# Kernel tuning notes

Hardware: AMD Instinct MI355X
Metric: run time of the kernel (lower is better)

Reference implementation:

```python
import jax, jax.numpy as jnp
import numpy as np

N_NODES = 50000
N_EDGES = 600000
IN_DIM = 128
HID_DIM = 256
LAT_DIM = 64


def setup_inputs() -> dict:
    key = jax.random.key(0)
    k_x, k_e, k_w1, k_b1, k_w2, k_b2 = jax.random.split(key, 6)
    x = jax.random.normal(k_x, (N_NODES, IN_DIM), dtype=jnp.float32)
    edge_index = jax.random.randint(k_e, (2, N_EDGES), 0, N_NODES, dtype=jnp.int64)
    # torch nn.Linear default init: U(-1/sqrt(fan_in), 1/sqrt(fan_in))
    lim1 = 1.0 / np.sqrt(2 * IN_DIM)
    lim2 = 1.0 / np.sqrt(HID_DIM)
    W1 = jax.random.uniform(k_w1, (2 * IN_DIM, HID_DIM), jnp.float32, -lim1, lim1)
    b1 = jax.random.uniform(k_b1, (HID_DIM,), jnp.float32, -lim1, lim1)
    W2 = jax.random.uniform(k_w2, (HID_DIM, LAT_DIM), jnp.float32, -lim2, lim2)
    b2 = jax.random.uniform(k_b2, (LAT_DIM,), jnp.float32, -lim2, lim2)
    return {"x": x, "edge_index": edge_index, "W1": W1, "b1": b1, "W2": W2, "b2": b2}


def reference(x, edge_index, W1, b1, W2, b2):
    h_i = x[edge_index[0]]                     # [E, D]
    h_j = x[edge_index[1]]                     # [E, D]
    edge_features = jnp.concatenate([h_i, h_j], axis=-1)  # [E, 2D]
    hidden = jax.nn.relu(edge_features @ W1 + b1)          # [E, H]
    return hidden @ W2 + b2                                # [E, L]
```

## Files before the change

### kernel.cpp

```cpp
#include <hip/hip_runtime.h>

#define E_TOTAL 600000
#define N_NODES 50000
#define NETILES 9375
#define NNT 782
#define LDS_X 136
#define LDP 264

typedef __attribute__((ext_vector_type(8))) short short8;
typedef __attribute__((ext_vector_type(8))) _Float16 half8;
typedef __attribute__((ext_vector_type(4))) float f32x4;

__device__ __forceinline__ unsigned f2bf_u(float f) {
  union { float f; unsigned u; } v; v.f = f;
  return (v.u + 0x7fffu + ((v.u >> 16) & 1u)) >> 16;
}
__device__ __forceinline__ unsigned short f2h_u(float f) {
  union { _Float16 h; unsigned short u; } v; v.h = (_Float16)f;
  return v.u;
}

__global__ __launch_bounds__(256) void prep(
    const float* __restrict__ W1, const float* __restrict__ W2,
    const float* __restrict__ b1,
    unsigned short* __restrict__ W1c, unsigned short* __restrict__ W2t2,
    unsigned short* __restrict__ b1h) {
  __shared__ float t[32][33];
  int bid = blockIdx.x;
  int tx = threadIdx.x & 31, ty = threadIdx.x >> 5;
  if (bid < 64) {
    int k0 = (bid >> 3) * 32, n0 = (bid & 7) * 32;
#pragma unroll
    for (int i = 0; i < 32; i += 8) t[ty + i][tx] = W1[(k0 + ty + i) * 256 + n0 + tx];
    __syncthreads();
    int coff = (k0 >= 128) ? 256 : 0;
#pragma unroll
    for (int i = 0; i < 32; i += 8)
      W1c[(n0 + ty + i + coff) * 128 + (k0 & 127) + tx] = (unsigned short)f2bf_u(t[tx][ty + i]);
  } else if (bid < 80) {
    int b = bid - 64;
    int k0 = (b >> 1) * 32, n0 = (b & 1) * 32;
#pragma unroll
    for (int i = 0; i < 32; i += 8) t[ty + i][tx] = W2[(k0 + ty + i) * 64 + n0 + tx];
    __syncthreads();
#pragma unroll
    for (int i = 0; i < 32; i += 8)
      W2t2[(n0 + ty + i) * 256 + k0 + tx] = f2h_u(t[tx][ty + i]);
  } else {
    b1h[threadIdx.x] = f2h_u(b1[threadIdx.x]);
  }
}

__global__ __launch_bounds__(256, 3) void node_uv(
    const float* __restrict__ x, const unsigned short* __restrict__ W1c,
    unsigned short* __restrict__ UV) {
  __shared__ __align__(16) unsigned short xt[64 * LDP];
  const int tid = threadIdx.x;
  const int ntile = (int)blockIdx.x >> 1, chalf = blockIdx.x & 1;
  const int n0 = ntile * 64;
  const int lane = tid & 63, w = tid >> 6, m = lane & 15, q = lane >> 4;

  const int kb = (tid & 15) * 8;
  const int r0 = tid >> 4;
#pragma unroll
  for (int i = 0; i < 4; ++i) {
    int r = r0 + 16 * i;
    int n = n0 + r; if (n >= N_NODES) n = N_NODES - 1;
    const float* p = x + (size_t)n * 128 + kb;
    f32x4 g0 = *(const f32x4*)p, g1 = *(const f32x4*)(p + 4);
    short8 s;
#pragma unroll
    for (int j = 0; j < 4; ++j) { s[j] = (short)f2bf_u(g0[j]); s[4 + j] = (short)f2bf_u(g1[j]); }
    *(short8*)&xt[r * LDS_X + kb] = s;
  }

  int w1o[4];
#pragma unroll
  for (int nt = 0; nt < 4; ++nt) w1o[nt] = (chalf * 256 + (w * 4 + nt) * 16 + m) * 128 + q * 8;
  short8 wa[2][4];
#pragma unroll
  for (int nt = 0; nt < 4; ++nt) wa[0][nt] = *(const short8*)&W1c[w1o[nt]];

  __syncthreads();

  f32x4 acc[4][4];
#pragma unroll
  for (int nt = 0; nt < 4; ++nt)
#pragma unroll
    for (int mt = 0; mt < 4; ++mt) acc[nt][mt] = (f32x4){0.f, 0.f, 0.f, 0.f};

#pragma unroll
  for (int kk = 0; kk < 4; ++kk) {
    const int cur = kk & 1, nx = cur ^ 1;
    if (kk < 3) {
#pragma unroll
      for (int nt = 0; nt < 4; ++nt) wa[nx][nt] = *(const short8*)&W1c[w1o[nt] + (kk + 1) * 32];
    }
    short8 f[4];
#pragma unroll
    for (int mt = 0; mt < 4; ++mt)
      f[mt] = *(const short8*)&xt[(mt * 16 + m) * LDS_X + kk * 32 + q * 8];
#pragma unroll
    for (int nt = 0; nt < 4; ++nt)
#pragma unroll
      for (int mt = 0; mt < 4; ++mt)
        acc[nt][mt] = __builtin_amdgcn_mfma_f32_16x16x32_bf16(wa[cur][nt], f[mt], acc[nt][mt], 0, 0, 0);
  }

  __syncthreads();

#pragma unroll
  for (int nt = 0; nt < 4; ++nt)
#pragma unroll
    for (int mt = 0; mt < 4; ++mt) {
      union { _Float16 h[4]; uint2 u; } pk;
#pragma unroll
      for (int r = 0; r < 4; ++r) pk.h[r] = (_Float16)acc[nt][mt][r];
      *(uint2*)&xt[(mt * 16 + m) * LDP + (w * 4 + nt) * 16 + q * 4] = pk.u;
    }

  __syncthreads();

  const int rr = tid >> 2, c8 = tid & 3;
  if (n0 + rr < N_NODES) {
    unsigned short* dst = UV + (size_t)(n0 + rr) * 512 + chalf * 256;
#pragma unroll
    for (int i = 0; i < 8; ++i) {
      int ch = c8 + 4 * i;
      *(short8*)&dst[ch * 8] = *(const short8*)&xt[rr * LDP + ch * 8];
    }
  }
}

__global__ __launch_bounds__(256, 4) void edge_mlp(
    const unsigned short* __restrict__ UV, const int* __restrict__ ei,
    const unsigned short* __restrict__ W2t2, const unsigned short* __restrict__ b1h,
    const float* __restrict__ b2, float* __restrict__ out) {
  __shared__ __align__(16) unsigned short hid[64 * LDP];
  const int tid = threadIdx.x;
  const int base = blockIdx.x * 64;
  const int lane = tid & 63, w = tid >> 6, m = lane & 15, q = lane >> 4;
  const int c = tid & 31;
  const int e0 = tid >> 5;

  half8 w2r[8];
  const int w2off = (w * 16 + m) * 256 + q * 8;
#pragma unroll
  for (int kk = 0; kk < 8; ++kk) w2r[kk] = *(const half8*)&W2t2[w2off + kk * 32];
  half8 bias = *(const half8*)&b1h[c * 8];
  f32x4 b2v = *(const f32x4*)&b2[w * 16 + q * 4];

  int si[8], di[8];
#pragma unroll
  for (int i = 0; i < 8; ++i) {
    int e = base + e0 + 8 * i;
    si[i] = ei[e];
    di[i] = ei[E_TOTAL + e];
  }

#pragma unroll
  for (int g = 0; g < 2; ++g) {
    half8 lu[4], lv[4];
#pragma unroll
    for (int i = 0; i < 4; ++i) {
      const int r = g * 4 + i;
      lu[i] = *(const half8*)&UV[(size_t)si[r] * 512 + c * 8];
      lv[i] = *(const half8*)&UV[(size_t)di[r] * 512 + 256 + c * 8];
    }
#pragma unroll
    for (int i = 0; i < 4; ++i) {
      const int r = g * 4 + i;
      half8 s = lu[i] + lv[i] + bias;
#pragma unroll
      for (int j = 0; j < 8; ++j) s[j] = s[j] > (_Float16)0 ? s[j] : (_Float16)0;
      *(half8*)&hid[(e0 + 8 * r) * LDP + c * 8] = s;
    }
  }

  __syncthreads();

  f32x4 acc2[4];
#pragma unroll
  for (int mt = 0; mt < 4; ++mt) acc2[mt] = (f32x4){0.f, 0.f, 0.f, 0.f};
#pragma unroll
  for (int kk = 0; kk < 8; ++kk) {
#pragma unroll
    for (int mt = 0; mt < 4; ++mt) {
      half8 h = *(const half8*)&hid[(mt * 16 + m) * LDP + kk * 32 + q * 8];
      acc2[mt] = __builtin_amdgcn_mfma_f32_16x16x32_f16(w2r[kk], h, acc2[mt], 0, 0, 0);
    }
  }

#pragma unroll
  for (int mt = 0; mt < 4; ++mt) {
    f32x4 o;
#pragma unroll
    for (int r = 0; r < 4; ++r) o[r] = acc2[mt][r] + b2v[r];
    __builtin_nontemporal_store(o, (f32x4*)&out[(size_t)(base + mt * 16 + m) * 64 + w * 16 + q * 4]);
  }
}

extern "C" void kernel_launch(void* const* d_in, const int* in_sizes, int n_in,
                              void* d_out, int out_size, void* d_ws, size_t ws_size,
                              hipStream_t stream) {
  const float* x  = (const float*)d_in[0];
  const int*   ei = (const int*)d_in[1];
  const float* W1 = (const float*)d_in[2];
  const float* b1 = (const float*)d_in[3];
  const float* W2 = (const float*)d_in[4];
  const float* b2 = (const float*)d_in[5];
  float* out = (float*)d_out;

  unsigned short* W1c  = (unsigned short*)d_ws;
  unsigned short* W2t2 = W1c + 512 * 128;
  unsigned short* b1h  = W2t2 + 64 * 256;
  unsigned short* UV   = b1h + 256;

  prep<<<81, 256, 0, stream>>>(W1, W2, b1, W1c, W2t2, b1h);
  node_uv<<<NNT * 2, 256, 0, stream>>>(x, W1c, UV);
  edge_mlp<<<NETILES, 256, 0, stream>>>(UV, ei, W2t2, b1h, b2, out);
}
```

Baseline: 290.9 us.

## Sort edges by source node to improve gather locality in edge MLP

Adds a counting sort of edges by source node (histogram, single-block scan, atomic scatter) and makes the edge kernel process edges in sorted order, writing outputs back through a permutation index. U and V are split into separate contiguous arrays so each gather hits a denser buffer. The aim is better cache reuse of source-node U rows during the random gather. In exchange it adds three kernels, one of which is a serial single-block scan, plus atomics and scattered output stores.

```diff
diff --git a/kernel.cpp b/kernel.cpp
--- a/kernel.cpp
+++ b/kernel.cpp
@@ -24,7 +24,7 @@
     const float* __restrict__ W1, const float* __restrict__ W2,
     const float* __restrict__ b1,
     unsigned short* __restrict__ W1c, unsigned short* __restrict__ W2t2,
-    unsigned short* __restrict__ b1h) {
+    unsigned short* __restrict__ b1h, int* __restrict__ hist) {
   __shared__ float t[32][33];
   int bid = blockIdx.x;
   int tx = threadIdx.x & 31, ty = threadIdx.x >> 5;
@@ -46,14 +46,54 @@
 #pragma unroll
     for (int i = 0; i < 32; i += 8)
       W2t2[(n0 + ty + i) * 256 + k0 + tx] = f2h_u(t[tx][ty + i]);
+  } else if (bid == 80) {
+    b1h[threadIdx.x] = f2h_u(b1[threadIdx.x]);
   } else {
-    b1h[threadIdx.x] = f2h_u(b1[threadIdx.x]);
+    int i = (bid - 81) * 256 + threadIdx.x;
+    if (i < N_NODES) hist[i] = 0;
+  }
+}
+
+__global__ __launch_bounds__(256) void ehist(const int* __restrict__ ei, int* __restrict__ hist) {
+  int e = blockIdx.x * 256 + threadIdx.x;
+  if (e < E_TOTAL) atomicAdd(&hist[ei[e]], 1);
+}
+
+__global__ __launch_bounds__(256) void escan(const int* __restrict__ hist, int* __restrict__ offs) {
+  __shared__ int tmp[256];
+  const int t = threadIdx.x;
+  const int b = t * 196;
+  int s = 0;
+#pragma unroll 4
+  for (int i = 0; i < 196; ++i) { int idx = b + i; if (idx < N_NODES) s += hist[idx]; }
+  tmp[t] = s; __syncthreads();
+  for (int o = 1; o < 256; o <<= 1) {
+    int v = (t >= o) ? tmp[t - o] : 0;
+    __syncthreads();
+    tmp[t] += v;
+    __syncthreads();
+  }
+  int run = tmp[t] - s;
+  for (int i = 0; i < 196; ++i) {
+    int idx = b + i;
+    if (idx < N_NODES) { offs[idx] = run; run += hist[idx]; }
+  }
+}
+
+__global__ __launch_bounds__(256) void escatter(const int* __restrict__ ei, int* __restrict__ offs,
+                                                int* __restrict__ ss, int* __restrict__ sd,
+                                                int* __restrict__ se) {
+  int e = blockIdx.x * 256 + threadIdx.x;
+  if (e < E_TOTAL) {
+    int s = ei[e], d = ei[E_TOTAL + e];
+    int p = atomicAdd(&offs[s], 1);
+    ss[p] = s; sd[p] = d; se[p] = e;
   }
 }
 
 __global__ __launch_bounds__(256, 3) void node_uv(
     const float* __restrict__ x, const unsigned short* __restrict__ W1c,
-    unsigned short* __restrict__ UV) {
+    unsigned short* __restrict__ U, unsigned short* __restrict__ V) {
   __shared__ __align__(16) unsigned short xt[64 * LDP];
   const int tid = threadIdx.x;
   const int ntile = (int)blockIdx.x >> 1, chalf = blockIdx.x & 1;
@@ -123,7 +163,7 @@
 
   const int rr = tid >> 2, c8 = tid & 3;
   if (n0 + rr < N_NODES) {
-    unsigned short* dst = UV + (size_t)(n0 + rr) * 512 + chalf * 256;
+    unsigned short* dst = (chalf ? V : U) + (size_t)(n0 + rr) * 256;
 #pragma unroll
     for (int i = 0; i < 8; ++i) {
       int ch = c8 + 4 * i;
@@ -133,7 +173,8 @@
 }
 
 __global__ __launch_bounds__(256, 4) void edge_mlp(
-    const unsigned short* __restrict__ UV, const int* __restrict__ ei,
+    const unsigned short* __restrict__ U, const unsigned short* __restrict__ V,
+    const int* __restrict__ ss, const int* __restrict__ sd, const int* __restrict__ se,
     const unsigned short* __restrict__ W2t2, const unsigned short* __restrict__ b1h,
     const float* __restrict__ b2, float* __restrict__ out) {
   __shared__ __align__(16) unsigned short hid[64 * LDP];
@@ -153,9 +194,9 @@
   int si[8], di[8];
 #pragma unroll
   for (int i = 0; i < 8; ++i) {
-    int e = base + e0 + 8 * i;
-    si[i] = ei[e];
-    di[i] = ei[E_TOTAL + e];
+    int r = base + e0 + 8 * i;
+    si[i] = ss[r];
+    di[i] = sd[r];
   }
 
 #pragma unroll
@@ -164,8 +205,8 @@
 #pragma unroll
     for (int i = 0; i < 4; ++i) {
       const int r = g * 4 + i;
-      lu[i] = *(const half8*)&UV[(size_t)si[r] * 512 + c * 8];
-      lv[i] = *(const half8*)&UV[(size_t)di[r] * 512 + 256 + c * 8];
+      lu[i] = *(const half8*)&U[(size_t)si[r] * 256 + c * 8];
+      lv[i] = *(const half8*)&V[(size_t)di[r] * 256 + c * 8];
     }
 #pragma unroll
     for (int i = 0; i < 4; ++i) {
@@ -193,10 +234,11 @@
 
 #pragma unroll
   for (int mt = 0; mt < 4; ++mt) {
+    int eo = se[base + mt * 16 + m];
     f32x4 o;
 #pragma unroll
     for (int r = 0; r < 4; ++r) o[r] = acc2[mt][r] + b2v[r];
-    __builtin_nontemporal_store(o, (f32x4*)&out[(size_t)(base + mt * 16 + m) * 64 + w * 16 + q * 4]);
+    __builtin_nontemporal_store(o, (f32x4*)&out[(size_t)eo * 64 + w * 16 + q * 4]);
   }
 }
 
@@ -214,9 +256,18 @@
   unsigned short* W1c  = (unsigned short*)d_ws;
   unsigned short* W2t2 = W1c + 512 * 128;
   unsigned short* b1h  = W2t2 + 64 * 256;
-  unsigned short* UV   = b1h + 256;
-
-  prep<<<81, 256, 0, stream>>>(W1, W2, b1, W1c, W2t2, b1h);
-  node_uv<<<NNT * 2, 256, 0, stream>>>(x, W1c, UV);
-  edge_mlp<<<NETILES, 256, 0, stream>>>(UV, ei, W2t2, b1h, b2, out);
-}
+  unsigned short* U    = b1h + 256;
+  unsigned short* V    = U + (size_t)N_NODES * 256;
+  int* hist = (int*)(V + (size_t)N_NODES * 256);
+  int* offs = hist + N_NODES;
+  int* ss   = offs + N_NODES;
+  int* sd   = ss + E_TOTAL;
+  int* se   = sd + E_TOTAL;
+
+  prep<<<277, 256, 0, stream>>>(W1, W2, b1, W1c, W2t2, b1h, hist);
+  ehist<<<2344, 256, 0, stream>>>(ei, hist);
+  escan<<<1, 256, 0, stream>>>(hist, offs);
+  escatter<<<2344, 256, 0, stream>>>(ei, offs, ss, sd, se);
+  node_uv<<<NNT * 2, 256, 0, stream>>>(x, W1c, U, V);
+  edge_mlp<<<NETILES, 256, 0, stream>>>(U, V, ss, sd, se, W2t2, b1h, b2, out);
+}
```

After: 427.4 us. 46.9% more time.

## Bucket-sort edges by source node to improve gather locality in edge MLP

Applied to the files above, without the earlier changes.

Adds a histogram, a single-block scan and an atomic scatter that bucket edges by source node (groups of 32), so the edge MLP gathers U rows with better cache locality. It also splits UV into separate U and V arrays and processes three 64-edge tiles per block, prefetching the next tile's gathers while the current one is computed. Outputs are written to the original edge positions, which turns the store into a scatter. The cost is extra kernels, atomics and a sorted buffer. Packing src and dst into 16 bits each relies on node ids fitting in 16 bits, which holds for 50000.

```diff
diff --git a/kernel.cpp b/kernel.cpp
--- a/kernel.cpp
+++ b/kernel.cpp
@@ -2,8 +2,11 @@
 
 #define E_TOTAL 600000
 #define N_NODES 50000
-#define NETILES 9375
+#define NBUCK 1563
+#define EB 3
+#define NEB 3125
 #define NNT 782
+#define SCAT_B 2344
 #define LDS_X 136
 #define LDP 264
 
@@ -19,14 +22,22 @@
   union { _Float16 h; unsigned short u; } v; v.h = (_Float16)f;
   return v.u;
 }
-
-__global__ __launch_bounds__(256) void prep(
+__device__ __forceinline__ void ldsBarrier() {
+  asm volatile("s_waitcnt lgkmcnt(0)\n\ts_barrier" ::: "memory");
+}
+
+__global__ __launch_bounds__(256) void prep_hist(
     const float* __restrict__ W1, const float* __restrict__ W2,
-    const float* __restrict__ b1,
+    const float* __restrict__ b1, const int* __restrict__ ei,
     unsigned short* __restrict__ W1c, unsigned short* __restrict__ W2t2,
-    unsigned short* __restrict__ b1h) {
+    unsigned short* __restrict__ b1h, int* __restrict__ hist) {
   __shared__ float t[32][33];
   int bid = blockIdx.x;
+  if (bid >= 81) {
+    int e = (bid - 81) * 256 + threadIdx.x;
+    if (e < E_TOTAL) atomicAdd(&hist[ei[e] >> 5], 1);
+    return;
+  }
   int tx = threadIdx.x & 31, ty = threadIdx.x >> 5;
   if (bid < 64) {
     int k0 = (bid >> 3) * 32, n0 = (bid & 7) * 32;
@@ -51,12 +62,52 @@
   }
 }
 
-__global__ __launch_bounds__(256, 3) void node_uv(
+__global__ __launch_bounds__(256) void bscan(const int* __restrict__ hist,
+                                             int* __restrict__ offs) {
+  __shared__ int tmp[256];
+  const int t = threadIdx.x;
+  const int base = t * 7;
+  int loc[7];
+  int s = 0;
+#pragma unroll
+  for (int i = 0; i < 7; ++i) {
+    int idx = base + i;
+    int v = (idx < NBUCK) ? hist[idx] : 0;
+    loc[i] = s; s += v;
+  }
+  tmp[t] = s; __syncthreads();
+  for (int o = 1; o < 256; o <<= 1) {
+    int u = (t >= o) ? tmp[t - o] : 0;
+    __syncthreads();
+    tmp[t] += u;
+    __syncthreads();
+  }
+  int pre = tmp[t] - s;
+#pragma unroll
+  for (int i = 0; i < 7; ++i) {
+    int idx = base + i;
+    if (idx < NBUCK) offs[idx] = pre + loc[i];
+  }
+}
+
+__global__ __launch_bounds__(256, 3) void scat_node(
+    const int* __restrict__ ei, int* __restrict__ offs, uint2* __restrict__ sorted,
     const float* __restrict__ x, const unsigned short* __restrict__ W1c,
-    unsigned short* __restrict__ UV) {
+    unsigned short* __restrict__ U, unsigned short* __restrict__ V) {
+  const int tid = threadIdx.x;
+  int bid = blockIdx.x;
+  if (bid < SCAT_B) {
+    int e = bid * 256 + tid;
+    if (e < E_TOTAL) {
+      int s = ei[e], d = ei[E_TOTAL + e];
+      int p = atomicAdd(&offs[s >> 5], 1);
+      sorted[p] = make_uint2((unsigned)s | ((unsigned)d << 16), (unsigned)e);
+    }
+    return;
+  }
   __shared__ __align__(16) unsigned short xt[64 * LDP];
-  const int tid = threadIdx.x;
-  const int ntile = (int)blockIdx.x >> 1, chalf = blockIdx.x & 1;
+  bid -= SCAT_B;
+  const int ntile = bid >> 1, chalf = bid & 1;
   const int n0 = ntile * 64;
   const int lane = tid & 63, w = tid >> 6, m = lane & 15, q = lane >> 4;
 
@@ -123,7 +174,7 @@
 
   const int rr = tid >> 2, c8 = tid & 3;
   if (n0 + rr < N_NODES) {
-    unsigned short* dst = UV + (size_t)(n0 + rr) * 512 + chalf * 256;
+    unsigned short* dst = (chalf ? V : U) + (size_t)(n0 + rr) * 256;
 #pragma unroll
     for (int i = 0; i < 8; ++i) {
       int ch = c8 + 4 * i;
@@ -132,13 +183,13 @@
   }
 }
 
-__global__ __launch_bounds__(256, 4) void edge_mlp(
-    const unsigned short* __restrict__ UV, const int* __restrict__ ei,
+__global__ __launch_bounds__(256, 3) void edge_mlp(
+    const unsigned short* __restrict__ U, const unsigned short* __restrict__ V,
+    const uint2* __restrict__ sorted,
     const unsigned short* __restrict__ W2t2, const unsigned short* __restrict__ b1h,
     const float* __restrict__ b2, float* __restrict__ out) {
   __shared__ __align__(16) unsigned short hid[64 * LDP];
   const int tid = threadIdx.x;
-  const int base = blockIdx.x * 64;
   const int lane = tid & 63, w = tid >> 6, m = lane & 15, q = lane >> 4;
   const int c = tid & 31;
   const int e0 = tid >> 5;
@@ -150,53 +201,61 @@
   half8 bias = *(const half8*)&b1h[c * 8];
   f32x4 b2v = *(const f32x4*)&b2[w * 16 + q * 4];
 
-  int si[8], di[8];
+  const int base = blockIdx.x * (EB * 64);
+
+  half8 gu[8], gv[8];
 #pragma unroll
   for (int i = 0; i < 8; ++i) {
-    int e = base + e0 + 8 * i;
-    si[i] = ei[e];
-    di[i] = ei[E_TOTAL + e];
-  }
-
-#pragma unroll
-  for (int g = 0; g < 2; ++g) {
-    half8 lu[4], lv[4];
-#pragma unroll
-    for (int i = 0; i < 4; ++i) {
-      const int r = g * 4 + i;
-      lu[i] = *(const half8*)&UV[(size_t)si[r] * 512 + c * 8];
-      lv[i] = *(const half8*)&UV[(size_t)di[r] * 512 + 256 + c * 8];
-    }
-#pragma unroll
-    for (int i = 0; i < 4; ++i) {
-      const int r = g * 4 + i;
-      half8 s = lu[i] + lv[i] + bias;
-#pragma unroll
-      for (int j = 0; j < 8; ++j) s[j] = s[j] > (_Float16)0 ? s[j] : (_Float16)0;
-      *(half8*)&hid[(e0 + 8 * r) * LDP + c * 8] = s;
-    }
-  }
-
-  __syncthreads();
-
-  f32x4 acc2[4];
-#pragma unroll
-  for (int mt = 0; mt < 4; ++mt) acc2[mt] = (f32x4){0.f, 0.f, 0.f, 0.f};
-#pragma unroll
-  for (int kk = 0; kk < 8; ++kk) {
+    uint2 s8 = sorted[base + e0 + 8 * i];
+    gu[i] = *(const half8*)&U[(size_t)(s8.x & 0xFFFFu) * 256 + c * 8];
+    gv[i] = *(const half8*)&V[(size_t)(s8.x >> 16) * 256 + c * 8];
+  }
+
+  for (int j = 0; j < EB; ++j) {
+    const int tb = base + j * 64;
+
+#pragma unroll
+    for (int i = 0; i < 8; ++i) {
+      half8 s = gu[i] + gv[i] + bias;
+#pragma unroll
+      for (int jj = 0; jj < 8; ++jj) s[jj] = s[jj] > (_Float16)0 ? s[jj] : (_Float16)0;
+      *(half8*)&hid[(e0 + 8 * i) * LDP + c * 8] = s;
+    }
+
+    if (j + 1 < EB) {
+      const int nb = tb + 64;
+#pragma unroll
+      for (int i = 0; i < 8; ++i) {
+        uint2 s8 = sorted[nb + e0 + 8 * i];
+        gu[i] = *(const half8*)&U[(size_t)(s8.x & 0xFFFFu) * 256 + c * 8];
+        gv[i] = *(const half8*)&V[(size_t)(s8.x >> 16) * 256 + c * 8];
+      }
+    }
+
+    ldsBarrier();
+
+    f32x4 acc2[4];
+#pragma unroll
+    for (int mt = 0; mt < 4; ++mt) acc2[mt] = (f32x4){0.f, 0.f, 0.f, 0.f};
+#pragma unroll
+    for (int kk = 0; kk < 8; ++kk) {
+#pragma unroll
+      for (int mt = 0; mt < 4; ++mt) {
+        half8 h = *(const half8*)&hid[(mt * 16 + m) * LDP + kk * 32 + q * 8];
+        acc2[mt] = __builtin_amdgcn_mfma_f32_16x16x32_f16(w2r[kk], h, acc2[mt], 0, 0, 0);
+      }
+    }
+
 #pragma unroll
     for (int mt = 0; mt < 4; ++mt) {
-      half8 h = *(const half8*)&hid[(mt * 16 + m) * LDP + kk * 32 + q * 8];
-      acc2[mt] = __builtin_amdgcn_mfma_f32_16x16x32_f16(w2r[kk], h, acc2[mt], 0, 0, 0);
-    }
-  }
-
-#pragma unroll
-  for (int mt = 0; mt < 4; ++mt) {
-    f32x4 o;
-#pragma unroll
-    for (int r = 0; r < 4; ++r) o[r] = acc2[mt][r] + b2v[r];
-    __builtin_nontemporal_store(o, (f32x4*)&out[(size_t)(base + mt * 16 + m) * 64 + w * 16 + q * 4]);
+      unsigned eo = sorted[tb + mt * 16 + m].y;
+      f32x4 o;
+#pragma unroll
+      for (int r = 0; r < 4; ++r) o[r] = acc2[mt][r] + b2v[r];
+      __builtin_nontemporal_store(o, (f32x4*)&out[(size_t)eo * 64 + w * 16 + q * 4]);
+    }
+
+    ldsBarrier();
   }
 }
 
@@ -214,9 +273,15 @@
   unsigned short* W1c  = (unsigned short*)d_ws;
   unsigned short* W2t2 = W1c + 512 * 128;
   unsigned short* b1h  = W2t2 + 64 * 256;
-  unsigned short* UV   = b1h + 256;
-
-  prep<<<81, 256, 0, stream>>>(W1, W2, b1, W1c, W2t2, b1h);
-  node_uv<<<NNT * 2, 256, 0, stream>>>(x, W1c, UV);
-  edge_mlp<<<NETILES, 256, 0, stream>>>(UV, ei, W2t2, b1h, b2, out);
-}
+  unsigned short* U    = b1h + 256;
+  unsigned short* V    = U + (size_t)N_NODES * 256;
+  int*   hist   = (int*)(V + (size_t)N_NODES * 256);
+  int*   offs   = hist + NBUCK;
+  uint2* sorted = (uint2*)(offs + NBUCK);
+
+  hipMemsetAsync(hist, 0, NBUCK * sizeof(int), stream);
+  prep_hist<<<81 + SCAT_B, 256, 0, stream>>>(W1, W2, b1, ei, W1c, W2t2, b1h, hist);
+  bscan<<<1, 256, 0, stream>>>(hist, offs);
+  scat_node<<<SCAT_B + NNT * 2, 256, 0, stream>>>(ei, offs, sorted, x, W1c, U, V);
+  edge_mlp<<<NEB, 256, 0, stream>>>(U, V, sorted, W2t2, b1h, b2, out);
+}
```

Measured after the change: 449.5 us. +54.5%, slower.
